# Optimization experiments

Measured on AMD Instinct MI355X. Metric: run time of the kernel, lower is better.

The kernel has to match this reference:

```python
import jax, jax.numpy as jnp
import numpy as np

N_NODES = 100000
N_EDGES = 1600000
D_IN = 480
D_OUT = 256
NEG_SLOPE = 0.2  # GATv2Conv default negative_slope


def setup_inputs() -> dict:
    key = jax.random.key(0)
    ks = jax.random.split(key, 8)
    s_in = 1.0 / np.sqrt(D_IN)
    s_out = 1.0 / np.sqrt(D_OUT)
    return {
        "x": jax.random.normal(ks[0], (N_NODES, D_IN), dtype=jnp.float32),
        "edge_index": jax.random.randint(ks[1], (2, N_EDGES), 0, N_NODES, dtype=jnp.int32),
        "W_l": jax.random.normal(ks[2], (D_IN, D_OUT), dtype=jnp.float32) * s_in,
        "b_l": jnp.zeros((D_OUT,), dtype=jnp.float32),
        "W_r": jax.random.normal(ks[3], (D_IN, D_OUT), dtype=jnp.float32) * s_in,
        "b_r": jnp.zeros((D_OUT,), dtype=jnp.float32),
        "att": jax.random.normal(ks[4], (D_OUT,), dtype=jnp.float32) * s_out,
        "bias": jnp.zeros((D_OUT,), dtype=jnp.float32),
    }


def reference(x, edge_index, W_l, b_l, W_r, b_r, att, bias):
    # Single GATv2Conv(480 -> 256, heads=1, concat=False), as built by
    # GAT(in=480, hidden=512, num_layers=1, out=256, v2=True, act='relu', norm=None)
    # (act is only applied between layers, so none here).
    src = edge_index[0]  # message source j
    dst = edge_index[1]  # aggregation target i

    x_l = x @ W_l + b_l  # [N, D_OUT] source-side transform
    x_r = x @ W_r + b_r  # [N, D_OUT] target-side transform

    # GATv2 attention logits: e_ij = att^T LeakyReLU(x_l[j] + x_r[i])
    h = x_l[src] + x_r[dst]                    # [E, D_OUT]
    h = jnp.where(h > 0, h, NEG_SLOPE * h)     # leaky_relu
    e = h @ att                                # [E]

    # segment softmax over incoming edges of each dst node (numerically stable)
    e_max = jax.ops.segment_max(e, dst, num_segments=N_NODES)
    e_max = jnp.where(jnp.isfinite(e_max), e_max, 0.0)  # nodes with no edges
    ex = jnp.exp(e - e_max[dst])                         # [E]
    denom = jax.ops.segment_sum(ex, dst, num_segments=N_NODES)
    alpha = ex / (denom[dst] + 1e-16)                    # PyG softmax eps

    # attention-weighted scatter-sum of source messages x_l[j]
    out = jax.ops.segment_sum(alpha[:, None] * x_l[src], dst, num_segments=N_NODES)
    return out + bias
```

## Files before the change

kernel.cpp:

```cpp
#include <hip/hip_runtime.h>
#include <hip/hip_bf16.h>

#define N_NODES 100000
#define N_EDGES 1600000
#define D_IN    480
#define D_OUT   256
#define NEG_SLOPE 0.2f
#define NKB     (D_IN / 32)

typedef __attribute__((ext_vector_type(8))) short bf16x8;
typedef __attribute__((ext_vector_type(4))) float f32x4;

__device__ __forceinline__ unsigned short f2bf_rn(float f) {
    unsigned u = __float_as_uint(f);
    return (unsigned short)((u + 0x7fffu + ((u >> 16) & 1u)) >> 16);
}

__device__ __forceinline__ void split_bf16(float f, unsigned short& h, unsigned short& l) {
    unsigned u  = __float_as_uint(f);
    unsigned hr = (u + 0x7fffu + ((u >> 16) & 1u)) >> 16;
    h = (unsigned short)hr;
    float fh = __uint_as_float(hr << 16);
    l = f2bf_rn(f - fh);
}

__global__ __launch_bounds__(256) void pack_w(
    const float* __restrict__ Wl, const float* __restrict__ Wr,
    unsigned short* __restrict__ whi, unsigned short* __restrict__ wlo)
{
    const int idx = blockIdx.x * 256 + threadIdx.x;
    if (idx >= D_IN * 512) return;
    const int k   = idx >> 9;
    const int col = idx & 511;
    const float f = (col < 256) ? Wl[(size_t)k * 256 + col]
                                : Wr[(size_t)k * 256 + (col - 256)];
    unsigned short h, l;
    split_bf16(f, h, l);
    const size_t o = ((size_t)((k >> 5) * 512 + col) << 5) | (size_t)(k & 31);
    whi[o] = h; wlo[o] = l;
}

__global__ __launch_bounds__(512) void gemm_mfma(
    const float* __restrict__ x,
    const unsigned short* __restrict__ whi,
    const unsigned short* __restrict__ wlo,
    const float* __restrict__ b_l, const float* __restrict__ b_r,
    float* __restrict__ yl, float* __restrict__ yr)
{
    __shared__ __align__(16) unsigned short Ahi[2][64 * 32];
    __shared__ __align__(16) unsigned short Alo[2][64 * 32];

    const int t    = threadIdx.x;
    const int wid  = t >> 6;
    const int lane = t & 63;
    const int r0   = blockIdx.x * 64;

    const int srow = t >> 3;
    const int sk4  = (t & 7) * 4;
    const int gr   = r0 + srow;
    const float* xrow   = x + (size_t)gr * D_IN;
    const bool  srow_ok = (gr < N_NODES);

    const int woff = srow * 32 + (((sk4 >> 3) ^ ((srow >> 1) & 3)) * 8) + (sk4 & 7);

    const int l15 = lane & 15;
    const int lg  = lane >> 4;

    int aoff[4];
    #pragma unroll
    for (int rf = 0; rf < 4; ++rf) {
        const int row = rf * 16 + l15;
        aoff[rf] = row * 32 + ((lg ^ ((row >> 1) & 3)) * 8);
    }

    f32x4 acc[4][4] = {};

    float4 xv  = make_float4(0.f, 0.f, 0.f, 0.f);
    float4 xq0 = make_float4(0.f, 0.f, 0.f, 0.f);
    float4 xq1 = make_float4(0.f, 0.f, 0.f, 0.f);
    if (srow_ok) {
        xv  = *(const float4*)(xrow + sk4);
        xq0 = *(const float4*)(xrow + 32 + sk4);
        xq1 = *(const float4*)(xrow + 64 + sk4);
    }
    {
        unsigned short h0,h1,h2,h3,l0,l1,l2,l3;
        split_bf16(xv.x, h0, l0); split_bf16(xv.y, h1, l1);
        split_bf16(xv.z, h2, l2); split_bf16(xv.w, h3, l3);
        *(uint2*)&Ahi[0][woff] = make_uint2((unsigned)h0 | ((unsigned)h1 << 16),
                                            (unsigned)h2 | ((unsigned)h3 << 16));
        *(uint2*)&Alo[0][woff] = make_uint2((unsigned)l0 | ((unsigned)l1 << 16),
                                            (unsigned)l2 | ((unsigned)l3 << 16));
    }
    asm volatile("s_waitcnt lgkmcnt(0)" ::: "memory");
    __builtin_amdgcn_s_barrier();
    __builtin_amdgcn_sched_barrier(0);

    for (int kb = 0; kb < NKB; ++kb) {
        const int p = kb & 1;

        const size_t bbase = ((size_t)kb * 512 + wid * 64 + l15) * 32 + lg * 8;
        bf16x8 bh[4], bl[4];
        #pragma unroll
        for (int cf = 0; cf < 4; ++cf) {
            bh[cf] = *(const bf16x8*)(whi + bbase + (size_t)cf * 512);
            bl[cf] = *(const bf16x8*)(wlo + bbase + (size_t)cf * 512);
        }

        bf16x8 ah[4], al[4];
        #pragma unroll
        for (int rf = 0; rf < 4; ++rf) {
            ah[rf] = *(const bf16x8*)&Ahi[p][aoff[rf]];
            al[rf] = *(const bf16x8*)&Alo[p][aoff[rf]];
        }

        if (kb + 1 < NKB) {
            unsigned short h0,h1,h2,h3,l0,l1,l2,l3;
            split_bf16(xq0.x, h0, l0); split_bf16(xq0.y, h1, l1);
            split_bf16(xq0.z, h2, l2); split_bf16(xq0.w, h3, l3);
            *(uint2*)&Ahi[p ^ 1][woff] = make_uint2((unsigned)h0 | ((unsigned)h1 << 16),
                                                    (unsigned)h2 | ((unsigned)h3 << 16));
            *(uint2*)&Alo[p ^ 1][woff] = make_uint2((unsigned)l0 | ((unsigned)l1 << 16),
                                                    (unsigned)l2 | ((unsigned)l3 << 16));
        }

        xq0 = xq1;
        if (kb + 3 < NKB && srow_ok)
            xq1 = *(const float4*)(xrow + (kb + 3) * 32 + sk4);

        __builtin_amdgcn_s_setprio(1);
        #pragma unroll
        for (int cf = 0; cf < 4; ++cf)
            #pragma unroll
            for (int rf = 0; rf < 4; ++rf)
                acc[rf][cf] = __builtin_amdgcn_mfma_f32_16x16x32_bf16(ah[rf], bh[cf], acc[rf][cf], 0, 0, 0);
        #pragma unroll
        for (int cf = 0; cf < 4; ++cf)
            #pragma unroll
            for (int rf = 0; rf < 4; ++rf)
                acc[rf][cf] = __builtin_amdgcn_mfma_f32_16x16x32_bf16(al[rf], bh[cf], acc[rf][cf], 0, 0, 0);
        #pragma unroll
        for (int cf = 0; cf < 4; ++cf)
            #pragma unroll
            for (int rf = 0; rf < 4; ++rf)
                acc[rf][cf] = __builtin_amdgcn_mfma_f32_16x16x32_bf16(ah[rf], bl[cf], acc[rf][cf], 0, 0, 0);
        __builtin_amdgcn_s_setprio(0);

        if (kb + 1 < NKB) {
            asm volatile("s_waitcnt lgkmcnt(0)" ::: "memory");
            __builtin_amdgcn_s_barrier();
            __builtin_amdgcn_sched_barrier(0);
        }
    }

    float* const y  = (wid < 4) ? yl : yr;
    const float* bp = (wid < 4) ? b_l : b_r;
    #pragma unroll
    for (int cf = 0; cf < 4; ++cf) {
        const int ocol  = (wid & 3) * 64 + cf * 16 + l15;
        const float bia = bp[ocol];
        #pragma unroll
        for (int rf = 0; rf < 4; ++rf) {
            const int row0 = r0 + rf * 16 + lg * 4;
            #pragma unroll
            for (int i = 0; i < 4; ++i) {
                if (row0 + i < N_NODES)
                    y[(size_t)(row0 + i) * D_OUT + ocol] = acc[rf][cf][i] + bia;
            }
        }
    }
}

__global__ void hist_k(const int* __restrict__ ei, unsigned* __restrict__ deg)
{
    const int e = blockIdx.x * 256 + threadIdx.x;
    if (e < N_EDGES) atomicAdd(&deg[ei[N_EDGES + e]], 1u);
}

__global__ void row_start_k(const unsigned* __restrict__ deg,
                            unsigned* __restrict__ row_start,
                            unsigned* __restrict__ cursor,
                            unsigned* __restrict__ total)
{
    const int i    = blockIdx.x * 256 + threadIdx.x;
    const int lane = threadIdx.x & 63;
    const unsigned d = (i < N_NODES) ? deg[i] : 0u;

    unsigned v = d;
    #pragma unroll
    for (int off = 1; off < 64; off <<= 1) {
        unsigned tt = __shfl_up(v, off, 64);
        if (lane >= off) v += tt;
    }
    const unsigned excl = v - d;
    const unsigned wave_total = __shfl(v, 63, 64);

    unsigned base = 0;
    if (lane == 0) base = atomicAdd(total, wave_total);
    base = __shfl(base, 0, 64);

    if (i < N_NODES) {
        row_start[i] = base + excl;
        cursor[i]    = base + excl;
    }
}

__global__ void scatter_k(const int* __restrict__ ei,
                          unsigned* __restrict__ cursor,
                          int* __restrict__ csr_src)
{
    const int e = blockIdx.x * 256 + threadIdx.x;
    if (e >= N_EDGES) return;
    const int dst = ei[N_EDGES + e];
    const unsigned pos = atomicAdd(&cursor[dst], 1u);
    csr_src[pos] = ei[e];
}

__global__ __launch_bounds__(256) void node_agg(
    const float* __restrict__ xl, const float* __restrict__ xr,
    const float* __restrict__ att, const int* __restrict__ csr_src,
    const unsigned* __restrict__ row_start, const unsigned* __restrict__ deg,
    const float* __restrict__ bias, float* __restrict__ out)
{
    const int node = (blockIdx.x * blockDim.x + threadIdx.x) >> 6;
    const int lane = threadIdx.x & 63;
    if (node >= N_NODES) return;

    const int start = (int)row_start[node];
    const int cnt   = (int)deg[node];
    const int end   = start + cnt;

    const float4 a  = *(const float4*)(att + lane * 4);
    const float4 r  = *(const float4*)(xr + (size_t)node * D_OUT + lane * 4);

    float  m = -INFINITY;
    float  s = 0.f;
    float4 acc = make_float4(0.f, 0.f, 0.f, 0.f);

#define LOGIT(LV, E) do { \
    float h0 = LV.x + r.x, h1 = LV.y + r.y, h2 = LV.z + r.z, h3 = LV.w + r.w; \
    h0 = h0 > 0.f ? h0 : NEG_SLOPE * h0; \
    h1 = h1 > 0.f ? h1 : NEG_SLOPE * h1; \
    h2 = h2 > 0.f ? h2 : NEG_SLOPE * h2; \
    h3 = h3 > 0.f ? h3 : NEG_SLOPE * h3; \
    E = h0 * a.x + h1 * a.y + h2 * a.z + h3 * a.w; \
} while (0)

#define ONE_EDGE(LV) do { \
    float e0; LOGIT(LV, e0); \
    _Pragma("unroll") \
    for (int off = 32; off > 0; off >>= 1) e0 += __shfl_xor(e0, off, 64); \
    const float m_new = fmaxf(m, e0); \
    const float sc    = __expf(m - m_new); \
    const float p0    = __expf(e0 - m_new); \
    s = s * sc + p0; \
    acc.x = acc.x * sc + p0 * LV.x; \
    acc.y = acc.y * sc + p0 * LV.y; \
    acc.z = acc.z * sc + p0 * LV.z; \
    acc.w = acc.w * sc + p0 * LV.w; \
    m = m_new; \
} while (0)

    float4 l0v = make_float4(0.f,0.f,0.f,0.f), l1v = l0v, l2v = l0v, l3v = l0v;
    if (start     < end) l0v = *(const float4*)(xl + (size_t)csr_src[start]     * D_OUT + lane * 4);
    if (start + 1 < end) l1v = *(const float4*)(xl + (size_t)csr_src[start + 1] * D_OUT + lane * 4);
    if (start + 2 < end) l2v = *(const float4*)(xl + (size_t)csr_src[start + 2] * D_OUT + lane * 4);
    if (start + 3 < end) l3v = *(const float4*)(xl + (size_t)csr_src[start + 3] * D_OUT + lane * 4);

    int j = start;
    for (; j + 3 < end; j += 4) {
        float4 n0 = make_float4(0.f,0.f,0.f,0.f), n1 = n0, n2 = n0, n3 = n0;
        if (j + 4 < end) n0 = *(const float4*)(xl + (size_t)csr_src[j + 4] * D_OUT + lane * 4);
        if (j + 5 < end) n1 = *(const float4*)(xl + (size_t)csr_src[j + 5] * D_OUT + lane * 4);
        if (j + 6 < end) n2 = *(const float4*)(xl + (size_t)csr_src[j + 6] * D_OUT + lane * 4);
        if (j + 7 < end) n3 = *(const float4*)(xl + (size_t)csr_src[j + 7] * D_OUT + lane * 4);

        float e0, e1, e2, e3;
        LOGIT(l0v, e0); LOGIT(l1v, e1); LOGIT(l2v, e2); LOGIT(l3v, e3);
        #pragma unroll
        for (int off = 32; off > 0; off >>= 1) {
            e0 += __shfl_xor(e0, off, 64);
            e1 += __shfl_xor(e1, off, 64);
            e2 += __shfl_xor(e2, off, 64);
            e3 += __shfl_xor(e3, off, 64);
        }

        const float m_new = fmaxf(fmaxf(fmaxf(m, e0), fmaxf(e1, e2)), e3);
        const float sc = __expf(m - m_new);
        const float p0 = __expf(e0 - m_new);
        const float p1 = __expf(e1 - m_new);
        const float p2 = __expf(e2 - m_new);
        const float p3 = __expf(e3 - m_new);
        s = s * sc + p0 + p1 + p2 + p3;
        acc.x = acc.x * sc + p0 * l0v.x + p1 * l1v.x + p2 * l2v.x + p3 * l3v.x;
        acc.y = acc.y * sc + p0 * l0v.y + p1 * l1v.y + p2 * l2v.y + p3 * l3v.y;
        acc.z = acc.z * sc + p0 * l0v.z + p1 * l1v.z + p2 * l2v.z + p3 * l3v.z;
        acc.w = acc.w * sc + p0 * l0v.w + p1 * l1v.w + p2 * l2v.w + p3 * l3v.w;
        m = m_new;

        l0v = n0; l1v = n1; l2v = n2; l3v = n3;
    }
    if (j < end) { ONE_EDGE(l0v); ++j; }
    if (j < end) { ONE_EDGE(l1v); ++j; }
    if (j < end) { ONE_EDGE(l2v); ++j; }

    const float inv = 1.f / (s + 1e-16f);
    const float4 bv = *(const float4*)(bias + lane * 4);
    float4 o;
    o.x = acc.x * inv + bv.x; o.y = acc.y * inv + bv.y;
    o.z = acc.z * inv + bv.z; o.w = acc.w * inv + bv.w;
    *(float4*)(out + (size_t)node * D_OUT + lane * 4) = o;

#undef ONE_EDGE
#undef LOGIT
}

extern "C" void kernel_launch(void* const* d_in, const int* in_sizes, int n_in,
                              void* d_out, int out_size, void* d_ws, size_t ws_size,
                              hipStream_t stream)
{
    const float* x   = (const float*)d_in[0];
    const int*   ei  = (const int*)  d_in[1];
    const float* W_l = (const float*)d_in[2];
    const float* b_l = (const float*)d_in[3];
    const float* W_r = (const float*)d_in[4];
    const float* b_r = (const float*)d_in[5];
    const float* att = (const float*)d_in[6];
    const float* bias= (const float*)d_in[7];
    float* out = (float*)d_out;

    float*    xl        = (float*)d_ws;
    float*    xr        = xl + (size_t)N_NODES * D_OUT;
    int*      csr_src   = (int*)(xr + (size_t)N_NODES * D_OUT);
    unsigned* deg       = (unsigned*)(csr_src + N_EDGES);
    unsigned* total     = deg + N_NODES;
    unsigned* row_start = total + 64;
    unsigned* cursor    = row_start + N_NODES;
    unsigned short* whi = (unsigned short*)(cursor + N_NODES);
    unsigned short* wlo = whi + (size_t)NKB * 512 * 32;

    pack_w<<<(D_IN * 512 + 255) / 256, 256, 0, stream>>>(W_l, W_r, whi, wlo);

    gemm_mfma<<<(N_NODES + 63) / 64, 512, 0, stream>>>(
        x, whi, wlo, b_l, b_r, xl, xr);

    hipMemsetAsync(deg, 0, (size_t)(N_NODES + 1) * sizeof(unsigned), stream);
    const int nb_nodes = (N_NODES + 255) / 256;
    const int nb_edges = (N_EDGES + 255) / 256;
    hist_k<<<nb_edges, 256, 0, stream>>>(ei, deg);
    row_start_k<<<nb_nodes, 256, 0, stream>>>(deg, row_start, cursor, total);
    scatter_k<<<nb_edges, 256, 0, stream>>>(ei, cursor, csr_src);

    node_agg<<<(N_NODES + 3) / 4, 256, 0, stream>>>(
        xl, xr, att, csr_src, row_start, deg, bias, out);
}
```

Measured before the change: 960.0 us.

## Prefetch weight fragments one k-step ahead and trim softmax reduction shuffles

In the projection GEMM, the bf16 hi/lo weight fragments for the next k-block are loaded into a register double buffer while the current block runs its MFMAs, and the k-loop is fully unrolled. This hides global load latency for B at the cost of more registers. In the aggregation kernel, the four per-edge logit reductions are packed into one butterfly, which cuts the cross-lane shuffles from 24 to about 11. The online-softmax rescale now only runs when the running max increases, and the CSR index is made wave-uniform with readfirstlane so the index loads can become scalar.

Result: no change. 945.3 us (-1.5%).

```diff
diff --git a/kernel.cpp b/kernel.cpp
--- a/kernel.cpp
+++ b/kernel.cpp
@@ -74,6 +74,9 @@
     }
 
     f32x4 acc[4][4] = {};
+    bf16x8 bhr[2][4], blr[2][4];
+
+    const size_t bfrag = ((size_t)wid * 64 + l15) * 32 + lg * 8;
 
     float4 xv  = make_float4(0.f, 0.f, 0.f, 0.f);
     float4 xq0 = make_float4(0.f, 0.f, 0.f, 0.f);
@@ -92,26 +95,34 @@
         *(uint2*)&Alo[0][woff] = make_uint2((unsigned)l0 | ((unsigned)l1 << 16),
                                             (unsigned)l2 | ((unsigned)l3 << 16));
     }
+    #pragma unroll
+    for (int cf = 0; cf < 4; ++cf) {
+        bhr[0][cf] = *(const bf16x8*)(whi + bfrag + (size_t)cf * 512);
+        blr[0][cf] = *(const bf16x8*)(wlo + bfrag + (size_t)cf * 512);
+    }
     asm volatile("s_waitcnt lgkmcnt(0)" ::: "memory");
     __builtin_amdgcn_s_barrier();
     __builtin_amdgcn_sched_barrier(0);
 
+    #pragma unroll
     for (int kb = 0; kb < NKB; ++kb) {
-        const int p = kb & 1;
-
-        const size_t bbase = ((size_t)kb * 512 + wid * 64 + l15) * 32 + lg * 8;
-        bf16x8 bh[4], bl[4];
-        #pragma unroll
-        for (int cf = 0; cf < 4; ++cf) {
-            bh[cf] = *(const bf16x8*)(whi + bbase + (size_t)cf * 512);
-            bl[cf] = *(const bf16x8*)(wlo + bbase + (size_t)cf * 512);
-        }
+        const int p  = kb & 1;
+        const int bp = kb & 1;
 
         bf16x8 ah[4], al[4];
         #pragma unroll
         for (int rf = 0; rf < 4; ++rf) {
             ah[rf] = *(const bf16x8*)&Ahi[p][aoff[rf]];
             al[rf] = *(const bf16x8*)&Alo[p][aoff[rf]];
+        }
+
+        if (kb + 1 < NKB) {
+            const size_t bb = (size_t)(kb + 1) * 512 * 32 + bfrag;
+            #pragma unroll
+            for (int cf = 0; cf < 4; ++cf) {
+                bhr[bp ^ 1][cf] = *(const bf16x8*)(whi + bb + (size_t)cf * 512);
+                blr[bp ^ 1][cf] = *(const bf16x8*)(wlo + bb + (size_t)cf * 512);
+            }
         }
 
         if (kb + 1 < NKB) {
@@ -133,17 +144,17 @@
         for (int cf = 0; cf < 4; ++cf)
             #pragma unroll
             for (int rf = 0; rf < 4; ++rf)
-                acc[rf][cf] = __builtin_amdgcn_mfma_f32_16x16x32_bf16(ah[rf], bh[cf], acc[rf][cf], 0, 0, 0);
+                acc[rf][cf] = __builtin_amdgcn_mfma_f32_16x16x32_bf16(ah[rf], bhr[bp][cf], acc[rf][cf], 0, 0, 0);
         #pragma unroll
         for (int cf = 0; cf < 4; ++cf)
             #pragma unroll
             for (int rf = 0; rf < 4; ++rf)
-                acc[rf][cf] = __builtin_amdgcn_mfma_f32_16x16x32_bf16(al[rf], bh[cf], acc[rf][cf], 0, 0, 0);
+                acc[rf][cf] = __builtin_amdgcn_mfma_f32_16x16x32_bf16(al[rf], bhr[bp][cf], acc[rf][cf], 0, 0, 0);
         #pragma unroll
         for (int cf = 0; cf < 4; ++cf)
             #pragma unroll
             for (int rf = 0; rf < 4; ++rf)
-                acc[rf][cf] = __builtin_amdgcn_mfma_f32_16x16x32_bf16(ah[rf], bl[cf], acc[rf][cf], 0, 0, 0);
+                acc[rf][cf] = __builtin_amdgcn_mfma_f32_16x16x32_bf16(ah[rf], blr[bp][cf], acc[rf][cf], 0, 0, 0);
         __builtin_amdgcn_s_setprio(0);
 
         if (kb + 1 < NKB) {
@@ -154,11 +165,11 @@
     }
 
     float* const y  = (wid < 4) ? yl : yr;
-    const float* bp = (wid < 4) ? b_l : b_r;
+    const float* bp2 = (wid < 4) ? b_l : b_r;
     #pragma unroll
     for (int cf = 0; cf < 4; ++cf) {
         const int ocol  = (wid & 3) * 64 + cf * 16 + l15;
-        const float bia = bp[ocol];
+        const float bia = bp2[ocol];
         #pragma unroll
         for (int rf = 0; rf < 4; ++rf) {
             const int row0 = r0 + rf * 16 + lg * 4;
@@ -251,14 +262,15 @@
     _Pragma("unroll") \
     for (int off = 32; off > 0; off >>= 1) e0 += __shfl_xor(e0, off, 64); \
     const float m_new = fmaxf(m, e0); \
-    const float sc    = __expf(m - m_new); \
-    const float p0    = __expf(e0 - m_new); \
-    s = s * sc + p0; \
-    acc.x = acc.x * sc + p0 * LV.x; \
-    acc.y = acc.y * sc + p0 * LV.y; \
-    acc.z = acc.z * sc + p0 * LV.z; \
-    acc.w = acc.w * sc + p0 * LV.w; \
-    m = m_new; \
+    if (m_new > m) { \
+        const float sc = __expf(m - m_new); \
+        s *= sc; acc.x *= sc; acc.y *= sc; acc.z *= sc; acc.w *= sc; \
+        m = m_new; \
+    } \
+    const float p0 = __expf(e0 - m); \
+    s += p0; \
+    acc.x += p0 * LV.x; acc.y += p0 * LV.y; \
+    acc.z += p0 * LV.z; acc.w += p0 * LV.w; \
 } while (0)
 
     float4 l0v = make_float4(0.f,0.f,0.f,0.f), l1v = l0v, l2v = l0v, l3v = l0v;
@@ -267,36 +279,60 @@
     if (start + 2 < end) l2v = *(const float4*)(xl + (size_t)csr_src[start + 2] * D_OUT + lane * 4);
     if (start + 3 < end) l3v = *(const float4*)(xl + (size_t)csr_src[start + 3] * D_OUT + lane * 4);
 
+    const int pb = lane & 1;
+    const int qb = lane & 2;
+    const int c  = lane & 3;
+
     int j = start;
     for (; j + 3 < end; j += 4) {
+        const int ju = __builtin_amdgcn_readfirstlane(j);
         float4 n0 = make_float4(0.f,0.f,0.f,0.f), n1 = n0, n2 = n0, n3 = n0;
-        if (j + 4 < end) n0 = *(const float4*)(xl + (size_t)csr_src[j + 4] * D_OUT + lane * 4);
-        if (j + 5 < end) n1 = *(const float4*)(xl + (size_t)csr_src[j + 5] * D_OUT + lane * 4);
-        if (j + 6 < end) n2 = *(const float4*)(xl + (size_t)csr_src[j + 6] * D_OUT + lane * 4);
-        if (j + 7 < end) n3 = *(const float4*)(xl + (size_t)csr_src[j + 7] * D_OUT + lane * 4);
+        if (j + 4 < end) n0 = *(const float4*)(xl + (size_t)csr_src[ju + 4] * D_OUT + lane * 4);
+        if (j + 5 < end) n1 = *(const float4*)(xl + (size_t)csr_src[ju + 5] * D_OUT + lane * 4);
+        if (j + 6 < end) n2 = *(const float4*)(xl + (size_t)csr_src[ju + 6] * D_OUT + lane * 4);
+        if (j + 7 < end) n3 = *(const float4*)(xl + (size_t)csr_src[ju + 7] * D_OUT + lane * 4);
 
         float e0, e1, e2, e3;
         LOGIT(l0v, e0); LOGIT(l1v, e1); LOGIT(l2v, e2); LOGIT(l3v, e3);
-        #pragma unroll
-        for (int off = 32; off > 0; off >>= 1) {
-            e0 += __shfl_xor(e0, off, 64);
-            e1 += __shfl_xor(e1, off, 64);
-            e2 += __shfl_xor(e2, off, 64);
-            e3 += __shfl_xor(e3, off, 64);
-        }
-
-        const float m_new = fmaxf(fmaxf(fmaxf(m, e0), fmaxf(e1, e2)), e3);
-        const float sc = __expf(m - m_new);
-        const float p0 = __expf(e0 - m_new);
-        const float p1 = __expf(e1 - m_new);
-        const float p2 = __expf(e2 - m_new);
-        const float p3 = __expf(e3 - m_new);
-        s = s * sc + p0 + p1 + p2 + p3;
-        acc.x = acc.x * sc + p0 * l0v.x + p1 * l1v.x + p2 * l2v.x + p3 * l3v.x;
-        acc.y = acc.y * sc + p0 * l0v.y + p1 * l1v.y + p2 * l2v.y + p3 * l3v.y;
-        acc.z = acc.z * sc + p0 * l0v.z + p1 * l1v.z + p2 * l2v.z + p3 * l3v.z;
-        acc.w = acc.w * sc + p0 * l0v.w + p1 * l1v.w + p2 * l2v.w + p3 * l3v.w;
-        m = m_new;
+
+        float z  = pb ? e1 : e0;
+        float zo = pb ? e0 : e1;
+        z += __shfl_xor(zo, 1, 64);
+        float w  = pb ? e3 : e2;
+        float wo = pb ? e2 : e3;
+        w += __shfl_xor(wo, 1, 64);
+        float v  = qb ? w : z;
+        float vo = qb ? z : w;
+        v += __shfl_xor(vo, 2, 64);
+        #pragma unroll
+        for (int off = 4; off < 64; off <<= 1) v += __shfl_xor(v, off, 64);
+        const float r1 = __shfl_xor(v, 1, 64);
+        const float r2 = __shfl_xor(v, 2, 64);
+        const float r3 = __shfl_xor(v, 3, 64);
+        const float t01  = pb ? r1 : v;
+        const float t01f = pb ? v  : r1;
+        const float t23  = pb ? r3 : r2;
+        const float t23f = pb ? r2 : r3;
+        const float S0 = qb ? t23  : t01;
+        const float S1 = qb ? t23f : t01f;
+        const float S2 = qb ? t01  : t23;
+        const float S3 = qb ? t01f : t23f;
+
+        const float m_new = fmaxf(m, fmaxf(fmaxf(v, r1), fmaxf(r2, r3)));
+        if (m_new > m) {
+            const float sc = __expf(m - m_new);
+            s *= sc; acc.x *= sc; acc.y *= sc; acc.z *= sc; acc.w *= sc;
+            m = m_new;
+        }
+        const float p0 = __expf(S0 - m);
+        const float p1 = __expf(S1 - m);
+        const float p2 = __expf(S2 - m);
+        const float p3 = __expf(S3 - m);
+        s += p0 + p1 + p2 + p3;
+        acc.x += p0 * l0v.x + p1 * l1v.x + p2 * l2v.x + p3 * l3v.x;
+        acc.y += p0 * l0v.y + p1 * l1v.y + p2 * l2v.y + p3 * l3v.y;
+        acc.z += p0 * l0v.z + p1 * l1v.z + p2 * l2v.z + p3 * l3v.z;
+        acc.w += p0 * l0v.w + p1 * l1v.w + p2 * l2v.w + p3 * l3v.w;
 
         l0v = n0; l1v = n1; l2v = n2; l3v = n3;
     }
```
